# Optimization experiments

Measured on AMD Instinct MI355X. Metric: run time of the kernel, lower is better.

Reference implementation:

```python
import jax, jax.numpy as jnp
import numpy as np

BATCH, FLAT_IN, PROJ_DIM, HEADS, ACT_DIM = 2048, 512, 256, 16384, 64


def setup_inputs() -> dict:
    key = jax.random.key(0)
    k1, k2, k3, k4 = jax.random.split(key, 4)
    state = jax.random.normal(k1, (BATCH, FLAT_IN), dtype=jnp.float32)
    random_projection = jax.random.normal(k2, (FLAT_IN, PROJ_DIM), dtype=jnp.float32)
    memories = jax.random.normal(k3, (HEADS, PROJ_DIM), dtype=jnp.float32)
    logits = jax.random.normal(k4, (HEADS, ACT_DIM), dtype=jnp.float32)
    return {"state": state, "random_projection": random_projection,
            "memories": memories, "logits": logits}


def reference(state, random_projection, memories, logits):
    # state: [B, flat_in] -> projected [B, proj_dim] (proj_dim branch of __call__)
    s = state.reshape(state.shape[0], -1) @ random_projection
    # sum(state[:,None] * memories[None,:], -1) == dot-product similarity GEMM
    similarities = jnp.einsum('bd,hd->bh', s, memories)  # [B, heads]
    closest = jnp.argmax(similarities, axis=1)           # [B]
    return logits[closest]                                # [B, act_dim]
```

## Files before the change

kernel.cpp:

```cpp
#include <hip/hip_runtime.h>

#define BATCH    2048
#define FLAT_IN  512
#define PROJ_DIM 256
#define HEADS    16384
#define ACT_DIM  64

typedef __attribute__((ext_vector_type(8))) short short8;
typedef _Float16 half8 __attribute__((ext_vector_type(8)));
typedef __attribute__((ext_vector_type(4))) float floatx4;

__device__ __forceinline__ unsigned short f2bf(float x) {
  unsigned u = __float_as_uint(x);
  u += 0x7fff + ((u >> 16) & 1);
  return (unsigned short)(u >> 16);
}
__device__ __forceinline__ float bf2f(unsigned short b) {
  return __uint_as_float(((unsigned)b) << 16);
}
__device__ __forceinline__ unsigned short f2h(float x) {
  _Float16 h = (_Float16)x;
  return __builtin_bit_cast(unsigned short, h);
}

__device__ __forceinline__ unsigned pack_key(float v, int h) {
  unsigned u = __float_as_uint(v);
  unsigned m = (unsigned)(((int)u) >> 31) | 0x80000000u;
  return ((u ^ m) & 0xFFFFC000u) | (unsigned)(16383 - h);
}

#define GLDS16(g, l)                                                          \
  __builtin_amdgcn_global_load_lds(                                           \
      (__attribute__((address_space(1))) void*)(void*)(g),                    \
      (__attribute__((address_space(3))) void*)(l), 16, 0, 0)

#define BARRIER() asm volatile("s_barrier" ::: "memory")

__global__ __launch_bounds__(256) void prep(
    const float* __restrict__ state, const float* __restrict__ rp,
    unsigned short* __restrict__ st_hi, unsigned short* __restrict__ st_mid,
    unsigned short* __restrict__ rpT_hi, unsigned short* __restrict__ rpT_mid)
{
  const int tid = threadIdx.x;
  const int b = blockIdx.x;
  if (b < 1024) {
    int i = b * 256 + tid;
    float4 v = ((const float4*)state)[i];
    ushort4 h, m;
    h.x = f2bf(v.x); m.x = f2bf(v.x - bf2f(h.x));
    h.y = f2bf(v.y); m.y = f2bf(v.y - bf2f(h.y));
    h.z = f2bf(v.z); m.z = f2bf(v.z - bf2f(h.z));
    h.w = f2bf(v.w); m.w = f2bf(v.w - bf2f(h.w));
    ((ushort4*)st_hi)[i]  = h;
    ((ushort4*)st_mid)[i] = m;
  } else {
    __shared__ float t[64][65];
    int bid = b - 1024;
    int k0 = (bid >> 2) * 64, n0 = (bid & 3) * 64;
#pragma unroll
    for (int it = 0; it < 16; ++it) {
      int lin = it * 256 + tid;
      int kr = lin >> 6, nc = lin & 63;
      t[kr][nc] = rp[(size_t)(k0 + kr) * PROJ_DIM + n0 + nc];
    }
    __syncthreads();
#pragma unroll
    for (int it = 0; it < 16; ++it) {
      int lin = it * 256 + tid;
      int nr = lin >> 6, kc = lin & 63;
      float v = t[kc][nr];
      unsigned short hh = f2bf(v);
      rpT_hi [(size_t)(n0 + nr) * FLAT_IN + k0 + kc] = hh;
      rpT_mid[(size_t)(n0 + nr) * FLAT_IN + k0 + kc] = f2bf(v - bf2f(hh));
    }
  }
}

__global__ __launch_bounds__(256, 2) void gemm_conv(
    const unsigned short* __restrict__ Ahi, const unsigned short* __restrict__ Amid,
    const unsigned short* __restrict__ Bhi, const unsigned short* __restrict__ Bmid,
    const float* __restrict__ mem,
    float* __restrict__ S, unsigned short* __restrict__ Sf16,
    unsigned short* __restrict__ mem_f16)
{
  const int tid = threadIdx.x;
  if (blockIdx.x >= 128) {
    int i2 = (blockIdx.x - 128) * 256 + tid;
    float4 x = ((const float4*)mem)[2 * i2];
    float4 y = ((const float4*)mem)[2 * i2 + 1];
    short8 o;
    o[0] = (short)f2h(x.x); o[1] = (short)f2h(x.y);
    o[2] = (short)f2h(x.z); o[3] = (short)f2h(x.w);
    o[4] = (short)f2h(y.x); o[5] = (short)f2h(y.y);
    o[6] = (short)f2h(y.z); o[7] = (short)f2h(y.w);
    __builtin_nontemporal_store(o, (short8*)mem_f16 + i2);
    return;
  }

  __shared__ __align__(16) unsigned short sm[4][64 * 64];
  const int lane = tid & 63, w = tid >> 6;
  const int quad = lane >> 4, col = lane & 15;
  const int wm = (w >> 1) * 32, wn = (w & 1) * 32;
  const int g = blockIdx.x;
  const int m0 = (g & 31) * 64, n0 = (g >> 5) * 64;

  floatx4 acc[2][2];
#pragma unroll
  for (int i = 0; i < 2; ++i)
#pragma unroll
    for (int j = 0; j < 2; ++j) {
      acc[i][j][0] = 0.f; acc[i][j][1] = 0.f;
      acc[i][j][2] = 0.f; acc[i][j][3] = 0.f;
    }

  const int P0 = tid, P1 = tid + 256;
  const int r0 = P0 >> 3, kl0 = (P0 & 7) ^ (r0 & 7);
  const int r1 = P1 >> 3, kl1 = (P1 & 7) ^ (r1 & 7);

  for (int kc = 0; kc < FLAT_IN; kc += 64) {
    GLDS16(Ahi  + (size_t)(m0 + r0) * FLAT_IN + kc + kl0 * 8, &sm[0][P0 * 8]);
    GLDS16(Ahi  + (size_t)(m0 + r1) * FLAT_IN + kc + kl1 * 8, &sm[0][P1 * 8]);
    GLDS16(Amid + (size_t)(m0 + r0) * FLAT_IN + kc + kl0 * 8, &sm[1][P0 * 8]);
    GLDS16(Amid + (size_t)(m0 + r1) * FLAT_IN + kc + kl1 * 8, &sm[1][P1 * 8]);
    GLDS16(Bhi  + (size_t)(n0 + r0) * FLAT_IN + kc + kl0 * 8, &sm[2][P0 * 8]);
    GLDS16(Bhi  + (size_t)(n0 + r1) * FLAT_IN + kc + kl1 * 8, &sm[2][P1 * 8]);
    GLDS16(Bmid + (size_t)(n0 + r0) * FLAT_IN + kc + kl0 * 8, &sm[3][P0 * 8]);
    GLDS16(Bmid + (size_t)(n0 + r1) * FLAT_IN + kc + kl1 * 8, &sm[3][P1 * 8]);
    __syncthreads();

#pragma unroll
    for (int ks = 0; ks < 2; ++ks) {
      short8 bf[2][2];
#pragma unroll
      for (int j = 0; j < 2; ++j) {
        int rr = wn + j * 16 + col;
        int off = rr * 64 + (((ks * 4 + quad) ^ (rr & 7)) * 8);
        bf[j][0] = *(const short8*)&sm[2][off];
        bf[j][1] = *(const short8*)&sm[3][off];
      }
#pragma unroll
      for (int i = 0; i < 2; ++i) {
        int rr = wm + i * 16 + col;
        int off = rr * 64 + (((ks * 4 + quad) ^ (rr & 7)) * 8);
        short8 a0 = *(const short8*)&sm[0][off];
        short8 a1 = *(const short8*)&sm[1][off];
#pragma unroll
        for (int j = 0; j < 2; ++j) {
          acc[i][j] = __builtin_amdgcn_mfma_f32_16x16x32_bf16(a0, bf[j][0], acc[i][j], 0, 0, 0);
          acc[i][j] = __builtin_amdgcn_mfma_f32_16x16x32_bf16(a0, bf[j][1], acc[i][j], 0, 0, 0);
          acc[i][j] = __builtin_amdgcn_mfma_f32_16x16x32_bf16(a1, bf[j][0], acc[i][j], 0, 0, 0);
        }
      }
    }
    __syncthreads();
  }

#pragma unroll
  for (int i = 0; i < 2; ++i)
#pragma unroll
    for (int j = 0; j < 2; ++j)
#pragma unroll
      for (int r = 0; r < 4; ++r) {
        int row = m0 + wm + i * 16 + quad * 4 + r;
        int c   = n0 + wn + j * 16 + col;
        float v = acc[i][j][r];
        S[(size_t)row * PROJ_DIM + c] = v;
        __builtin_nontemporal_store(f2h(v), Sf16 + (size_t)row * PROJ_DIM + c);
      }
}

__global__ __launch_bounds__(512, 2) void sim_topk(
    const unsigned short* __restrict__ Af16,
    const unsigned short* __restrict__ Bf16,
    unsigned* __restrict__ part1)
{
  __shared__ __align__(16) unsigned short smA[2][256 * 64];
  __shared__ __align__(16) unsigned short smB[2][256 * 64];
  const int tid = threadIdx.x;
  const int lane = tid & 63, w = tid >> 6;
  const int quad = lane >> 4, col = lane & 15;
  const int wm = (w >> 2) * 128, wn = (w & 3) * 64;

  const int bswz = blockIdx.x;
  const int xg   = bswz & 7;
  const int memb = bswz >> 3;
  const int hc   = xg * 8 + (memb & 7);
  const int mb   = memb >> 3;
  const int h0 = hc * 256;
  const int m0 = mb * 256;

  floatx4 acc[8][4];
#pragma unroll
  for (int i = 0; i < 8; ++i)
#pragma unroll
    for (int j = 0; j < 4; ++j) {
      acc[i][j][0] = 0.f; acc[i][j][1] = 0.f;
      acc[i][j][2] = 0.f; acc[i][j][3] = 0.f;
    }

  int rs[4], kl[4];
#pragma unroll
  for (int t = 0; t < 4; ++t) {
    int P = t * 512 + tid;
    rs[t] = P >> 3; kl[t] = (P & 7) ^ (rs[t] & 7);
  }

#define STAGE_KT(kt)                                                          \
  do {                                                                        \
    const int _kc = (kt) * 64;                                                \
    _Pragma("unroll")                                                         \
    for (int t = 0; t < 4; ++t)                                               \
      GLDS16(Af16 + (size_t)(m0 + rs[t]) * PROJ_DIM + _kc + kl[t] * 8,        \
             &smA[(kt) & 1][(t * 512 + tid) * 8]);                            \
    _Pragma("unroll")                                                         \
    for (int t = 0; t < 4; ++t)                                               \
      GLDS16(Bf16 + (size_t)(h0 + rs[t]) * PROJ_DIM + _kc + kl[t] * 8,        \
             &smB[(kt) & 1][(t * 512 + tid) * 8]);                            \
  } while (0)

  STAGE_KT(0);

#pragma unroll
  for (int kt = 0; kt < 4; ++kt) {
    if (kt < 3) {
      STAGE_KT(kt + 1);
      asm volatile("s_waitcnt vmcnt(8)" ::: "memory");
    } else {
      asm volatile("s_waitcnt vmcnt(0)" ::: "memory");
    }
    BARRIER();
    __builtin_amdgcn_sched_barrier(0);

    const unsigned short* A = smA[kt & 1];
    const unsigned short* B = smB[kt & 1];
#pragma unroll
    for (int ks = 0; ks < 2; ++ks) {
      half8 a[8], bfr[4];
#pragma unroll
      for (int j = 0; j < 4; ++j) {
        int rr = wn + j * 16 + col;
        int off = rr * 64 + (((ks * 4 + quad) ^ (rr & 7)) * 8);
        bfr[j] = *(const half8*)&B[off];
      }
#pragma unroll
      for (int i = 0; i < 8; ++i) {
        int rr = wm + i * 16 + col;
        int off = rr * 64 + (((ks * 4 + quad) ^ (rr & 7)) * 8);
        a[i] = *(const half8*)&A[off];
      }
#pragma unroll
      for (int i = 0; i < 8; ++i)
#pragma unroll
        for (int j = 0; j < 4; ++j)
          acc[i][j] = __builtin_amdgcn_mfma_f32_16x16x32_f16(a[i], bfr[j], acc[i][j], 0, 0, 0);
    }

    if (kt < 3) {
      asm volatile("s_waitcnt lgkmcnt(0)" ::: "memory");
      BARRIER();
    }
  }
#undef STAGE_KT

#pragma unroll
  for (int i = 0; i < 8; ++i)
#pragma unroll
    for (int r = 0; r < 4; ++r) {
      unsigned best = pack_key(acc[i][0][r], h0 + wn + col);
#pragma unroll
      for (int j = 1; j < 4; ++j) {
        unsigned k = pack_key(acc[i][j][r], h0 + wn + j * 16 + col);
        best = best > k ? best : k;
      }
#pragma unroll
      for (int m = 1; m <= 8; m <<= 1) {
        unsigned o = (unsigned)__shfl_xor((int)best, m);
        best = best > o ? best : o;
      }
      if (col == 0) {
        int row = m0 + wm + i * 16 + quad * 4 + r;
        part1[((size_t)row * 64 + hc) * 4 + (w & 3)] = best;
      }
    }
}

__global__ __launch_bounds__(64) void finalize(
    const unsigned* __restrict__ part1, const float* __restrict__ S,
    const float* __restrict__ Mem, const float* __restrict__ logits,
    float* __restrict__ out)
{
  const int row  = blockIdx.x;
  const int lane = threadIdx.x;

  unsigned k[4];
#pragma unroll
  for (int t = 0; t < 4; ++t)
    k[t] = part1[(size_t)row * 256 + t * 64 + lane];

  int cand[4]; float4 mv[4];
#pragma unroll
  for (int t = 0; t < 4; ++t) {
    unsigned lv = k[0];
#pragma unroll
    for (int q = 1; q < 4; ++q) lv = lv > k[q] ? lv : k[q];
#pragma unroll
    for (int d = 32; d; d >>= 1) {
      unsigned o = (unsigned)__shfl_xor((int)lv, d);
      lv = lv > o ? lv : o;
    }
    cand[t] = 16383 - (int)(lv & 16383u);
    mv[t] = ((const float4*)(Mem + (size_t)cand[t] * PROJ_DIM))[lane];
#pragma unroll
    for (int q = 0; q < 4; ++q)
      if (k[q] == lv) k[q] = 0;
  }

  float4 sv = ((const float4*)(S + (size_t)row * PROJ_DIM))[lane];
  float bestv = -3.4e38f; int besth = 0x7fffffff;
#pragma unroll
  for (int t = 0; t < 4; ++t) {
    float d = sv.x * mv[t].x + sv.y * mv[t].y + sv.z * mv[t].z + sv.w * mv[t].w;
#pragma unroll
    for (int s = 32; s; s >>= 1) d += __shfl_xor(d, s);
    if (d > bestv || (d == bestv && cand[t] < besth)) { bestv = d; besth = cand[t]; }
  }
  out[(size_t)row * ACT_DIM + lane] = logits[(size_t)besth * ACT_DIM + lane];
}

extern "C" void kernel_launch(void* const* d_in, const int* in_sizes, int n_in,
                              void* d_out, int out_size, void* d_ws, size_t ws_size,
                              hipStream_t stream) {
  const float* state  = (const float*)d_in[0];
  const float* rp     = (const float*)d_in[1];
  const float* mem    = (const float*)d_in[2];
  const float* logits = (const float*)d_in[3];
  float* out = (float*)d_out;

  char* ws = (char*)d_ws;
  unsigned short* st_hi   = (unsigned short*)(ws);
  unsigned short* st_mid  = (unsigned short*)(ws + (2u  << 20));
  unsigned short* rpT_hi  = (unsigned short*)(ws + (4u  << 20));
  unsigned short* rpT_mid = (unsigned short*)(ws + (4u  << 20) + (256u << 10));
  unsigned short* mem_f16 = (unsigned short*)(ws + (8u  << 20));
  float*          s       = (float*)(ws + (16u << 20));
  unsigned short* s_f16   = (unsigned short*)(ws + (18u << 20));
  unsigned*       part1   = (unsigned*)(ws + (20u << 20));

  prep<<<1056, 256, 0, stream>>>(state, rp, st_hi, st_mid, rpT_hi, rpT_mid);

  gemm_conv<<<2176, 256, 0, stream>>>(st_hi, st_mid, rpT_hi, rpT_mid, mem,
                                      s, s_f16, mem_f16);

  sim_topk<<<512, 512, 0, stream>>>(s_f16, mem_f16, part1);

  finalize<<<BATCH, 64, 0, stream>>>(part1, s, mem, logits, out);
}
```

Before: 116.7 us.

## Process two M tiles per sim_topk block with cross-tile prefetch

Each sim_topk block now handles two 256-row batch tiles (mbb and mbb+4) for the same memory head chunk. The grid is halved to 256 blocks, and the first K-tile of the second M tile is prefetched during the last K step of the first. This is meant to amortize launch and prologue costs and keep the load pipeline busy across tiles. The trade-off is fewer blocks (256 on a GPU with many CUs), which may lower occupancy and leave some CUs idle.

Result: no change. 118.6 us (+1.6%).

```diff
diff --git a/kernel.cpp b/kernel.cpp
--- a/kernel.cpp
+++ b/kernel.cpp
@@ -181,13 +181,14 @@
   const int quad = lane >> 4, col = lane & 15;
   const int wm = (w >> 2) * 128, wn = (w & 3) * 64;
 
-  const int bswz = blockIdx.x;
-  const int xg   = bswz & 7;
-  const int memb = bswz >> 3;
+  const int b    = blockIdx.x;
+  const int xg   = b & 7;
+  const int memb = b >> 3;
   const int hc   = xg * 8 + (memb & 7);
-  const int mb   = memb >> 3;
-  const int h0 = hc * 256;
-  const int m0 = mb * 256;
+  const int mbb  = memb >> 3;
+  const int h0   = hc * 256;
+  const int m0_0 = mbb * 256;
+  const int m0_1 = (mbb + 4) * 256;
 
   floatx4 acc[8][4];
 #pragma unroll
@@ -205,12 +206,12 @@
     rs[t] = P >> 3; kl[t] = (P & 7) ^ (rs[t] & 7);
   }
 
-#define STAGE_KT(kt)                                                          \
+#define STAGE_KT(m0x, kt)                                                     \
   do {                                                                        \
     const int _kc = (kt) * 64;                                                \
     _Pragma("unroll")                                                         \
     for (int t = 0; t < 4; ++t)                                               \
-      GLDS16(Af16 + (size_t)(m0 + rs[t]) * PROJ_DIM + _kc + kl[t] * 8,        \
+      GLDS16(Af16 + (size_t)((m0x) + rs[t]) * PROJ_DIM + _kc + kl[t] * 8,     \
              &smA[(kt) & 1][(t * 512 + tid) * 8]);                            \
     _Pragma("unroll")                                                         \
     for (int t = 0; t < 4; ++t)                                               \
@@ -218,70 +219,88 @@
              &smB[(kt) & 1][(t * 512 + tid) * 8]);                            \
   } while (0)
 
-  STAGE_KT(0);
-
-#pragma unroll
-  for (int kt = 0; kt < 4; ++kt) {
-    if (kt < 3) {
-      STAGE_KT(kt + 1);
-      asm volatile("s_waitcnt vmcnt(8)" ::: "memory");
-    } else {
-      asm volatile("s_waitcnt vmcnt(0)" ::: "memory");
-    }
-    BARRIER();
-    __builtin_amdgcn_sched_barrier(0);
-
-    const unsigned short* A = smA[kt & 1];
-    const unsigned short* B = smB[kt & 1];
-#pragma unroll
-    for (int ks = 0; ks < 2; ++ks) {
-      half8 a[8], bfr[4];
-#pragma unroll
-      for (int j = 0; j < 4; ++j) {
-        int rr = wn + j * 16 + col;
-        int off = rr * 64 + (((ks * 4 + quad) ^ (rr & 7)) * 8);
-        bfr[j] = *(const half8*)&B[off];
-      }
-#pragma unroll
-      for (int i = 0; i < 8; ++i) {
-        int rr = wm + i * 16 + col;
-        int off = rr * 64 + (((ks * 4 + quad) ^ (rr & 7)) * 8);
-        a[i] = *(const half8*)&A[off];
-      }
+  STAGE_KT(m0_0, 0);
+
+#pragma unroll
+  for (int T = 0; T < 2; ++T) {
+    const int m0 = T ? m0_1 : m0_0;
+
+#pragma unroll
+    for (int kt = 0; kt < 4; ++kt) {
+      if (kt < 3) {
+        STAGE_KT(m0, kt + 1);
+        asm volatile("s_waitcnt vmcnt(8)" ::: "memory");
+      } else if (T == 0) {
+        STAGE_KT(m0_1, 0);
+        asm volatile("s_waitcnt vmcnt(8)" ::: "memory");
+      } else {
+        asm volatile("s_waitcnt vmcnt(0)" ::: "memory");
+      }
+      BARRIER();
+      __builtin_amdgcn_sched_barrier(0);
+
+      const unsigned short* A = smA[kt & 1];
+      const unsigned short* B = smB[kt & 1];
+#pragma unroll
+      for (int ks = 0; ks < 2; ++ks) {
+        half8 a[8], bfr[4];
+#pragma unroll
+        for (int j = 0; j < 4; ++j) {
+          int rr = wn + j * 16 + col;
+          int off = rr * 64 + (((ks * 4 + quad) ^ (rr & 7)) * 8);
+          bfr[j] = *(const half8*)&B[off];
+        }
+#pragma unroll
+        for (int i = 0; i < 8; ++i) {
+          int rr = wm + i * 16 + col;
+          int off = rr * 64 + (((ks * 4 + quad) ^ (rr & 7)) * 8);
+          a[i] = *(const half8*)&A[off];
+        }
+#pragma unroll
+        for (int i = 0; i < 8; ++i)
+#pragma unroll
+          for (int j = 0; j < 4; ++j)
+            acc[i][j] = __builtin_amdgcn_mfma_f32_16x16x32_f16(a[i], bfr[j], acc[i][j], 0, 0, 0);
+      }
+
+      if (!(T == 1 && kt == 3)) {
+        asm volatile("s_waitcnt lgkmcnt(0)" ::: "memory");
+        BARRIER();
+      }
+    }
+
+#pragma unroll
+    for (int i = 0; i < 8; ++i)
+#pragma unroll
+      for (int r = 0; r < 4; ++r) {
+        unsigned best = pack_key(acc[i][0][r], h0 + wn + col);
+#pragma unroll
+        for (int j = 1; j < 4; ++j) {
+          unsigned k = pack_key(acc[i][j][r], h0 + wn + j * 16 + col);
+          best = best > k ? best : k;
+        }
+#pragma unroll
+        for (int m = 1; m <= 8; m <<= 1) {
+          unsigned o = (unsigned)__shfl_xor((int)best, m);
+          best = best > o ? best : o;
+        }
+        if (col == 0) {
+          int row = m0 + wm + i * 16 + quad * 4 + r;
+          part1[((size_t)row * 64 + hc) * 4 + (w & 3)] = best;
+        }
+      }
+
+    if (T == 0) {
 #pragma unroll
       for (int i = 0; i < 8; ++i)
 #pragma unroll
-        for (int j = 0; j < 4; ++j)
-          acc[i][j] = __builtin_amdgcn_mfma_f32_16x16x32_f16(a[i], bfr[j], acc[i][j], 0, 0, 0);
-    }
-
-    if (kt < 3) {
-      asm volatile("s_waitcnt lgkmcnt(0)" ::: "memory");
-      BARRIER();
+        for (int j = 0; j < 4; ++j) {
+          acc[i][j][0] = 0.f; acc[i][j][1] = 0.f;
+          acc[i][j][2] = 0.f; acc[i][j][3] = 0.f;
+        }
     }
   }
 #undef STAGE_KT
-
-#pragma unroll
-  for (int i = 0; i < 8; ++i)
-#pragma unroll
-    for (int r = 0; r < 4; ++r) {
-      unsigned best = pack_key(acc[i][0][r], h0 + wn + col);
-#pragma unroll
-      for (int j = 1; j < 4; ++j) {
-        unsigned k = pack_key(acc[i][j][r], h0 + wn + j * 16 + col);
-        best = best > k ? best : k;
-      }
-#pragma unroll
-      for (int m = 1; m <= 8; m <<= 1) {
-        unsigned o = (unsigned)__shfl_xor((int)best, m);
-        best = best > o ? best : o;
-      }
-      if (col == 0) {
-        int row = m0 + wm + i * 16 + quad * 4 + r;
-        part1[((size_t)row * 64 + hc) * 4 + (w & 3)] = best;
-      }
-    }
 }
 
 __global__ __launch_bounds__(64) void finalize(
@@ -351,7 +370,7 @@
   gemm_conv<<<2176, 256, 0, stream>>>(st_hi, st_mid, rpT_hi, rpT_mid, mem,
                                       s, s_f16, mem_f16);
 
-  sim_topk<<<512, 512, 0, stream>>>(s_f16, mem_f16, part1);
+  sim_topk<<<256, 512, 0, stream>>>(s_f16, mem_f16, part1);
 
   finalize<<<BATCH, 64, 0, stream>>>(part1, s, mem, logits, out);
 }
```
